# Kernel optimization log

Measured on AMD Instinct MI355X. Metric: run time of the kernel, lower is better.

Reference implementation:

```python
import jax, jax.numpy as jnp
import numpy as np

B, N, DIM, H = 8, 1024, 512, 8
D = DIM // H
SCALE = DIM ** -0.5


def setup_inputs() -> dict:
    key = jax.random.key(0)
    ks = jax.random.split(key, 8)
    s = 0.02
    return {
        "x": jax.random.normal(ks[0], (B, N, DIM), dtype=jnp.float32),
        "mask": jax.random.uniform(ks[1], (1, 1, N, N), dtype=jnp.float32),
        "Wqkv1": jax.random.normal(ks[2], (DIM, 3 * DIM), dtype=jnp.float32) * s,
        "bqkv1": jnp.zeros((3 * DIM,), dtype=jnp.float32),
        "Wqkv2": jax.random.normal(ks[3], (DIM, 3 * DIM), dtype=jnp.float32) * s,
        "bqkv2": jnp.zeros((3 * DIM,), dtype=jnp.float32),
        "Wnn1": jax.random.normal(ks[4], (DIM, DIM), dtype=jnp.float32) * s,
        "bnn1": jnp.zeros((DIM,), dtype=jnp.float32),
    }


def _split_heads(qkv, b, n):
    # qkv: [b, n, 3*dim] -> three [b, h, n, d]
    q, k, v = jnp.split(qkv, 3, axis=-1)
    r = lambda t: t.reshape(b, n, H, D).transpose(0, 2, 1, 3)
    return r(q), r(k), r(v)


def reference(x, mask, Wqkv1, bqkv1, Wqkv2, bqkv2, Wnn1, bnn1):
    b, n, dim = x.shape
    # Stage 1: mask-scaled sigmoid attention (no softmax, no scale)
    q, k, v = _split_heads(x @ Wqkv1 + bqkv1, b, n)
    dots = jax.nn.sigmoid(jnp.einsum('bhid,bhjd->bhij', q, k) * mask)
    out1 = jnp.einsum('bhij,bhjd->bhid', dots, v)
    out1 = out1.transpose(0, 2, 1, 3).reshape(b, n, dim)
    # Stage 2: standard scaled softmax attention on stage-1 output
    q, k, v = _split_heads(out1 @ Wqkv2 + bqkv2, b, n)
    attn = jax.nn.softmax(jnp.einsum('bhid,bhjd->bhij', q, k) * SCALE, axis=-1)
    out = jnp.einsum('bhij,bhjd->bhid', attn, v)
    out = out.transpose(0, 2, 1, 3).reshape(b, n, dim)
    # Output projection (dropout is identity in eval mode)
    return out @ Wnn1 + bnn1
```

## Files before the change

### kernel.cpp

```cpp
#include <hip/hip_runtime.h>
#include <hip/hip_bf16.h>
#include <stdint.h>

constexpr int B_ = 8, N_ = 1024, DIM_ = 512, H_ = 8, D_ = 64;
constexpr int BH_ = B_ * H_;
constexpr int M_  = B_ * N_;
constexpr float SCALE_ = 0.04419417382415922f;
constexpr float LOG2E_ = 1.44269504088896f;
constexpr float QSL2E_ = SCALE_ * LOG2E_;

typedef __bf16 bf16x8 __attribute__((ext_vector_type(8)));
typedef float  f32x4  __attribute__((ext_vector_type(4)));
typedef unsigned short u16;
typedef u16 u16x8 __attribute__((ext_vector_type(8)));
typedef u16 u16x4 __attribute__((ext_vector_type(4)));

static __device__ __forceinline__ u16 f2bf(float f) {
  return __builtin_bit_cast(u16, (__bf16)f);
}
static __device__ __forceinline__ bf16x8 ld8(const u16* p) {
  return __builtin_bit_cast(bf16x8, *reinterpret_cast<const u16x8*>(p));
}
static __device__ __forceinline__ f32x4 mfma16(bf16x8 a, bf16x8 b, f32x4 c) {
  return __builtin_amdgcn_mfma_f32_16x16x32_bf16(a, b, c, 0, 0, 0);
}
static __device__ __forceinline__ void gload_lds16(const u16* g, void* l) {
  __builtin_amdgcn_global_load_lds(
      (const __attribute__((address_space(1))) void*)g,
      (__attribute__((address_space(3))) void*)l, 16, 0, 0);
}

__global__ void k_cvt(const float* __restrict__ in, u16* __restrict__ out, int n4) {
  int i = blockIdx.x * blockDim.x + threadIdx.x;
  int stride = gridDim.x * blockDim.x;
  for (int idx = i; idx < n4; idx += stride) {
    float4 v = reinterpret_cast<const float4*>(in)[idx];
    u16x4 o;
    o[0] = f2bf(v.x); o[1] = f2bf(v.y); o[2] = f2bf(v.z); o[3] = f2bf(v.w);
    reinterpret_cast<u16x4*>(out)[idx] = o;
  }
}

__global__ void k_mask(const float* __restrict__ in, float* __restrict__ out, int n4) {
  int i = blockIdx.x * blockDim.x + threadIdx.x;
  int stride = gridDim.x * blockDim.x;
  for (int idx = i; idx < n4; idx += stride) {
    float4 v = reinterpret_cast<const float4*>(in)[idx];
    v.x *= -LOG2E_; v.y *= -LOG2E_; v.z *= -LOG2E_; v.w *= -LOG2E_;
    reinterpret_cast<float4*>(out)[idx] = v;
  }
}

__global__ void k_wt(const float* __restrict__ W, u16* __restrict__ Wt, int ncols, float qs) {
  int idx = blockIdx.x * 256 + threadIdx.x;
  if (idx >= ncols * 512) return;
  int c = idx >> 9, k = idx & 511;
  float v = W[k * ncols + c];
  if (c < 512) v *= qs;
  Wt[idx] = f2bf(v);
}

template<int NC, int MODE, bool SQ>
__global__ __launch_bounds__(256) void k_gemm(
    const u16* __restrict__ A, const u16* __restrict__ Wt, const float* __restrict__ bias,
    u16* __restrict__ qo, u16* __restrict__ ko, u16* __restrict__ vto, float* __restrict__ fo)
{
  __shared__ __attribute__((aligned(16))) u16 As[2][128 * 32];
  __shared__ __attribute__((aligned(16))) u16 Bs[2][128 * 32];
  const int wv = threadIdx.x >> 6, ln = threadIdx.x & 63;
  const int lr = ln & 15, lg = ln >> 4;
  const int wr = wv >> 1, wc = wv & 1;
  const int r0 = blockIdx.x * 128;
  const int c0 = blockIdx.y * 128;

  auto stage = [&](int bufi, int kk) {
#pragma unroll
    for (int q = 0; q < 2; ++q) {
      int L = (wv * 2 + q) * 1024 + ln * 16;
      int row = L >> 6;
      int col = ((L & 63) ^ (((row >> 1) & 3) << 4)) >> 1;
      gload_lds16(A  + (size_t)(r0 + row) * 512 + kk + col, (char*)As[bufi] + (wv * 2 + q) * 1024);
      gload_lds16(Wt + (size_t)(c0 + row) * 512 + kk + col, (char*)Bs[bufi] + (wv * 2 + q) * 1024);
    }
  };
  auto swzld = [&](const u16* tile, int row, int colb) -> bf16x8 {
    int byte = (row << 6) + (colb ^ (((row >> 1) & 3) << 4));
    return __builtin_bit_cast(bf16x8, *reinterpret_cast<const u16x8*>((const char*)tile + byte));
  };

  f32x4 acc[4][4] = {};
  stage(0, 0);
  int buf = 0;
  for (int kk = 0; kk < 512; kk += 32) {
    __syncthreads();
    if (kk + 32 < 512) stage(buf ^ 1, kk + 32);
    bf16x8 af[4], bfb[4];
#pragma unroll
    for (int m = 0; m < 4; ++m) af[m]  = swzld(As[buf], wr * 64 + m * 16 + lr, lg * 16);
#pragma unroll
    for (int n = 0; n < 4; ++n) bfb[n] = swzld(Bs[buf], wc * 64 + n * 16 + lr, lg * 16);
#pragma unroll
    for (int m = 0; m < 4; ++m)
#pragma unroll
      for (int n = 0; n < 4; ++n)
        acc[m][n] = mfma16(af[m], bfb[n], acc[m][n]);
    buf ^= 1;
  }

#pragma unroll
  for (int m = 0; m < 4; ++m)
#pragma unroll
    for (int n = 0; n < 4; ++n) {
      const int gc  = c0 + wc * 64 + n * 16 + lr;
      const int gr0 = r0 + wr * 64 + m * 16 + lg * 4;
      const float bsc = (SQ && gc < 512) ? QSL2E_ : 1.f;
      const float bv = bias[gc] * bsc;
      if (MODE == 0) {
        const int part = gc >> 9, cc = gc & 511;
        const int hh = cc >> 6, dd = cc & 63;
        const int bb = gr0 >> 10, nn = gr0 & 1023;
        const int bh = bb * H_ + hh;
        if (part == 2) {
          u16x4 w;
#pragma unroll
          for (int r = 0; r < 4; ++r) w[r] = f2bf(acc[m][n][r] + bv);
          *reinterpret_cast<u16x4*>(&vto[((size_t)(bh * D_ + dd)) * N_ + nn]) = w;
        } else {
          u16* dst = (part == 0 ? qo : ko) + ((size_t)(bh * N_ + nn)) * D_ + dd;
#pragma unroll
          for (int r = 0; r < 4; ++r) dst[(size_t)r * D_] = f2bf(acc[m][n][r] + bv);
        }
      } else {
#pragma unroll
        for (int r = 0; r < 4; ++r)
          fo[(size_t)(gr0 + r) * NC + gc] = acc[m][n][r] + bv;
      }
    }
}

template<int STAGE>
__global__ __launch_bounds__(512, 4) void k_attn(
    const u16* __restrict__ Q, const u16* __restrict__ K, const u16* __restrict__ Vt,
    const float* __restrict__ mask, u16* __restrict__ O)
{
  __shared__ __attribute__((aligned(16))) u16 Kb[2][64 * 64];
  __shared__ __attribute__((aligned(16))) u16 Vb[2][64 * 64];
  __shared__ __attribute__((aligned(16))) u16 pbuf[8][16][72];
  const int wv = threadIdx.x >> 6, ln = threadIdx.x & 63;
  const int lr = ln & 15, lg = ln >> 4;
  const int bh = blockIdx.y;
  const int i0 = blockIdx.x * 128 + wv * 16;
  const size_t base = (size_t)bh * N_ * D_;

  auto stageKV = [&](int bufi, int jt2) {
    int L = wv * 1024 + ln * 16;
    int row = L >> 7;
    int col = ((L & 127) ^ ((row & 7) << 4)) >> 1;
    gload_lds16(K  + base + (size_t)(jt2 + row) * 64 + col,  (char*)Kb[bufi] + wv * 1024);
    gload_lds16(Vt + base + (size_t)row * 1024 + jt2 + col,  (char*)Vb[bufi] + wv * 1024);
  };
  auto swzld = [&](const u16* tile, int row, int colb) -> bf16x8 {
    int byte = (row << 7) + (colb ^ ((row & 7) << 4));
    return __builtin_bit_cast(bf16x8, *reinterpret_cast<const u16x8*>((const char*)tile + byte));
  };

  bf16x8 aq0 = ld8(Q + base + (size_t)(i0 + lr) * D_ + lg * 8);
  bf16x8 aq1 = ld8(Q + base + (size_t)(i0 + lr) * D_ + 32 + lg * 8);

  f32x4 acco[4] = {};
  float ssum_ln = 0.f;

  float4 mk[4];
  const float* mrow = mask + (size_t)(i0 + lr) * N_;
  auto loadmask = [&](int jt2) {
#pragma unroll
    for (int js = 0; js < 4; ++js)
      mk[js] = *reinterpret_cast<const float4*>(&mrow[jt2 + js * 16 + lg * 4]);
  };
  if (STAGE == 1) loadmask(0);

  stageKV(0, 0);
  int buf = 0;
  for (int jt = 0; jt < N_; jt += 64) {
    __syncthreads();
    if (jt + 64 < N_) stageKV(buf ^ 1, jt + 64);

    f32x4 s[4];
    __builtin_amdgcn_s_setprio(1);
#pragma unroll
    for (int js = 0; js < 4; ++js) {
      int krow = js * 16 + lr;
      bf16x8 bk0 = swzld(Kb[buf], krow, lg * 16);
      bf16x8 bk1 = swzld(Kb[buf], krow, 64 + lg * 16);
      f32x4 z = {};
      z = mfma16(bk0, aq0, z);
      z = mfma16(bk1, aq1, z);
      s[js] = z;
    }
    __builtin_amdgcn_s_setprio(0);

    if (STAGE == 1) {
#pragma unroll
      for (int js = 0; js < 4; ++js) {
        u16x4 w;
#pragma unroll
        for (int r = 0; r < 4; ++r) {
          float mkr = (r == 0) ? mk[js].x : (r == 1) ? mk[js].y : (r == 2) ? mk[js].z : mk[js].w;
          float e = exp2f(s[js][r] * mkr);
          w[r] = f2bf(__builtin_amdgcn_rcpf(1.f + e));
        }
        *reinterpret_cast<u16x4*>(&pbuf[wv][lr][js * 16 + lg * 4]) = w;
      }
      if (jt + 64 < N_) loadmask(jt + 64);
    } else {
      float ps = 0.f;
#pragma unroll
      for (int js = 0; js < 4; ++js) {
        u16x4 w;
#pragma unroll
        for (int r = 0; r < 4; ++r) {
          float p = exp2f(s[js][r]);
          ps += p;
          w[r] = f2bf(p);
        }
        *reinterpret_cast<u16x4*>(&pbuf[wv][lr][js * 16 + lg * 4]) = w;
      }
      ssum_ln += ps;
    }

    bf16x8 ap0 = ld8(&pbuf[wv][lr][lg * 8]);
    bf16x8 ap1 = ld8(&pbuf[wv][lr][32 + lg * 8]);
    __builtin_amdgcn_s_setprio(1);
#pragma unroll
    for (int db = 0; db < 4; ++db) {
      bf16x8 bv0 = swzld(Vb[buf], db * 16 + lr, lg * 16);
      bf16x8 bv1 = swzld(Vb[buf], db * 16 + lr, 64 + lg * 16);
      acco[db] = mfma16(ap1, bv1, mfma16(ap0, bv0, acco[db]));
    }
    __builtin_amdgcn_s_setprio(0);
    buf ^= 1;
  }

  float inv[4];
  if (STAGE == 2) {
    float st = ssum_ln;
    st += __shfl_xor(st, 16);
    st += __shfl_xor(st, 32);
#pragma unroll
    for (int r = 0; r < 4; ++r)
      inv[r] = __builtin_amdgcn_rcpf(__shfl(st, lg * 4 + r));
  }

#pragma unroll
  for (int db = 0; db < 4; ++db)
#pragma unroll
    for (int r = 0; r < 4; ++r) {
      float v = acco[db][r];
      if (STAGE == 2) v *= inv[r];
      pbuf[wv][lg * 4 + r][db * 16 + lr] = f2bf(v);
    }
  bf16x8 o0v = ld8(&pbuf[wv][lr][lg * 8]);
  bf16x8 o1v = ld8(&pbuf[wv][lr][32 + lg * 8]);
  const int bb = bh >> 3, hh = bh & 7;
  u16* orow = O + (size_t)(bb * N_ + i0 + lr) * DIM_ + hh * D_;
  *reinterpret_cast<u16x8*>(orow + lg * 8)      = __builtin_bit_cast(u16x8, o0v);
  *reinterpret_cast<u16x8*>(orow + 32 + lg * 8) = __builtin_bit_cast(u16x8, o1v);
}

extern "C" void kernel_launch(void* const* d_in, const int* in_sizes, int n_in,
                              void* d_out, int out_size, void* d_ws, size_t ws_size,
                              hipStream_t stream)
{
  const float* x    = (const float*)d_in[0];
  const float* mask = (const float*)d_in[1];
  const float* W1   = (const float*)d_in[2];
  const float* b1   = (const float*)d_in[3];
  const float* W2   = (const float*)d_in[4];
  const float* b2   = (const float*)d_in[5];
  const float* W3   = (const float*)d_in[6];
  const float* b3   = (const float*)d_in[7];
  float* out = (float*)d_out;

  char* ws = (char*)d_ws;
  size_t off = 0;
  auto alloc = [&](size_t bytes) { char* p = ws + off; off += (bytes + 255) & ~255ULL; return p; };
  u16*   W1t = (u16*)alloc((size_t)1536 * 512 * 2);
  u16*   W2t = (u16*)alloc((size_t)1536 * 512 * 2);
  u16*   W3t = (u16*)alloc((size_t)512 * 512 * 2);
  u16*   xb  = (u16*)alloc((size_t)M_ * DIM_ * 2);
  u16*   q   = (u16*)alloc((size_t)BH_ * N_ * D_ * 2);
  u16*   k   = (u16*)alloc((size_t)BH_ * N_ * D_ * 2);
  u16*   vt  = (u16*)alloc((size_t)BH_ * N_ * D_ * 2);
  u16*   o1  = (u16*)alloc((size_t)M_ * DIM_ * 2);
  float* mk  = (float*)alloc((size_t)N_ * N_ * 4);
  u16*   o2  = xb;

  k_cvt<<<2048, 256, 0, stream>>>(x, xb, M_ * DIM_ / 4);
  k_mask<<<1024, 256, 0, stream>>>(mask, mk, N_ * N_ / 4);
  k_wt<<<(1536 * 512 + 255) / 256, 256, 0, stream>>>(W1, W1t, 1536, 1.f);
  k_wt<<<(1536 * 512 + 255) / 256, 256, 0, stream>>>(W2, W2t, 1536, QSL2E_);
  k_wt<<<(512 * 512 + 255) / 256, 256, 0, stream>>>(W3, W3t, 512, 1.f);

  dim3 g1(M_ / 128, 1536 / 128);
  k_gemm<1536, 0, false><<<g1, 256, 0, stream>>>(xb, W1t, b1, q, k, vt, nullptr);

  dim3 ga(N_ / 128, BH_);
  k_attn<1><<<ga, 512, 0, stream>>>(q, k, vt, mk, o1);

  k_gemm<1536, 0, true><<<g1, 256, 0, stream>>>(o1, W2t, b2, q, k, vt, nullptr);

  k_attn<2><<<ga, 512, 0, stream>>>(q, k, vt, mk, o2);

  dim3 g3(M_ / 128, 512 / 128);
  k_gemm<512, 1, false><<<g3, 256, 0, stream>>>(o2, W3t, b3, nullptr, nullptr, nullptr, out);
}
```

Before: 228.5 us.

## Fuse prep kernels into one launch with tiled weight transpose and GEMM block swizzle

Replaces the five preprocessing launches (x conversion, mask scaling, three weight transposes) with one kernel whose block ranges handle each job. The weight transpose now goes through a padded 64x64 shared-memory tile, so global reads and writes are coalesced instead of strided. The GEMM also remaps block indices with an XCD-style swizzle so that neighbouring blocks share A/B tiles in cache. The swizzle hardcodes 64 row tiles (M/128), which holds for every GEMM launch here.

Result: no change. 225.3 us (-1.4%).

```diff
diff --git a/kernel.cpp b/kernel.cpp
--- a/kernel.cpp
+++ b/kernel.cpp
@@ -30,34 +30,52 @@
       (__attribute__((address_space(3))) void*)l, 16, 0, 0);
 }
 
-__global__ void k_cvt(const float* __restrict__ in, u16* __restrict__ out, int n4) {
-  int i = blockIdx.x * blockDim.x + threadIdx.x;
-  int stride = gridDim.x * blockDim.x;
-  for (int idx = i; idx < n4; idx += stride) {
-    float4 v = reinterpret_cast<const float4*>(in)[idx];
-    u16x4 o;
-    o[0] = f2bf(v.x); o[1] = f2bf(v.y); o[2] = f2bf(v.z); o[3] = f2bf(v.w);
-    reinterpret_cast<u16x4*>(out)[idx] = o;
+__global__ __launch_bounds__(256) void k_prep(
+    const float* __restrict__ x, const float* __restrict__ mask,
+    const float* __restrict__ W1, const float* __restrict__ W2,
+    const float* __restrict__ W3,
+    u16* __restrict__ xb, float* __restrict__ mk,
+    u16* __restrict__ W1t, u16* __restrict__ W2t, u16* __restrict__ W3t)
+{
+  __shared__ float fl[64][65];
+  const int b = blockIdx.x, t = threadIdx.x;
+  if (b < 4096) {
+    int idx = b * 256 + t;
+    float4 v = reinterpret_cast<const float4*>(x)[idx];
+    u16x4 o; o[0] = f2bf(v.x); o[1] = f2bf(v.y); o[2] = f2bf(v.z); o[3] = f2bf(v.w);
+    reinterpret_cast<u16x4*>(xb)[idx] = o;
+  } else if (b < 5120) {
+    int idx = (b - 4096) * 256 + t;
+    float4 v = reinterpret_cast<const float4*>(mask)[idx];
+    v.x *= -LOG2E_; v.y *= -LOG2E_; v.z *= -LOG2E_; v.w *= -LOG2E_;
+    reinterpret_cast<float4*>(mk)[idx] = v;
+  } else {
+    int tb = b - 5120;
+    const float* Ws; u16* Wd; int NC, kt, ct; bool isW2 = false;
+    if (tb < 192)      { Ws = W1; Wd = W1t; NC = 1536; kt = tb / 24; ct = tb % 24; }
+    else if (tb < 384) { tb -= 192; Ws = W2; Wd = W2t; NC = 1536; kt = tb / 24; ct = tb % 24; isW2 = true; }
+    else               { tb -= 384; Ws = W3; Wd = W3t; NC = 512;  kt = tb >> 3; ct = tb & 7; }
+    const int tr = t >> 4, tc = t & 15;
+#pragma unroll
+    for (int i = 0; i < 4; ++i) {
+      int row = i * 16 + tr;
+      float4 v = *reinterpret_cast<const float4*>(
+          &Ws[(size_t)(kt * 64 + row) * NC + ct * 64 + tc * 4]);
+      fl[row][tc * 4 + 0] = v.x; fl[row][tc * 4 + 1] = v.y;
+      fl[row][tc * 4 + 2] = v.z; fl[row][tc * 4 + 3] = v.w;
+    }
+    __syncthreads();
+#pragma unroll
+    for (int i = 0; i < 4; ++i) {
+      int wr = i * 16 + tr;
+      int c = ct * 64 + wr;
+      float sc = (isW2 && c < 512) ? QSL2E_ : 1.f;
+      u16x4 w;
+#pragma unroll
+      for (int e = 0; e < 4; ++e) w[e] = f2bf(fl[tc * 4 + e][wr] * sc);
+      *reinterpret_cast<u16x4*>(&Wd[(size_t)c * 512 + kt * 64 + tc * 4]) = w;
+    }
   }
-}
-
-__global__ void k_mask(const float* __restrict__ in, float* __restrict__ out, int n4) {
-  int i = blockIdx.x * blockDim.x + threadIdx.x;
-  int stride = gridDim.x * blockDim.x;
-  for (int idx = i; idx < n4; idx += stride) {
-    float4 v = reinterpret_cast<const float4*>(in)[idx];
-    v.x *= -LOG2E_; v.y *= -LOG2E_; v.z *= -LOG2E_; v.w *= -LOG2E_;
-    reinterpret_cast<float4*>(out)[idx] = v;
-  }
-}
-
-__global__ void k_wt(const float* __restrict__ W, u16* __restrict__ Wt, int ncols, float qs) {
-  int idx = blockIdx.x * 256 + threadIdx.x;
-  if (idx >= ncols * 512) return;
-  int c = idx >> 9, k = idx & 511;
-  float v = W[k * ncols + c];
-  if (c < 512) v *= qs;
-  Wt[idx] = f2bf(v);
 }
 
 template<int NC, int MODE, bool SQ>
@@ -70,8 +88,11 @@
   const int wv = threadIdx.x >> 6, ln = threadIdx.x & 63;
   const int lr = ln & 15, lg = ln >> 4;
   const int wr = wv >> 1, wc = wv & 1;
-  const int r0 = blockIdx.x * 128;
-  const int c0 = blockIdx.y * 128;
+  const int nwg = gridDim.x * gridDim.y;
+  const int lin = blockIdx.y * gridDim.x + blockIdx.x;
+  const int swz = (lin & 7) * (nwg >> 3) + (lin >> 3);
+  const int r0 = (swz & 63) * 128;
+  const int c0 = (swz >> 6) * 128;
 
   auto stage = [&](int bufi, int kk) {
 #pragma unroll
@@ -295,11 +316,7 @@
   float* mk  = (float*)alloc((size_t)N_ * N_ * 4);
   u16*   o2  = xb;
 
-  k_cvt<<<2048, 256, 0, stream>>>(x, xb, M_ * DIM_ / 4);
-  k_mask<<<1024, 256, 0, stream>>>(mask, mk, N_ * N_ / 4);
-  k_wt<<<(1536 * 512 + 255) / 256, 256, 0, stream>>>(W1, W1t, 1536, 1.f);
-  k_wt<<<(1536 * 512 + 255) / 256, 256, 0, stream>>>(W2, W2t, 1536, QSL2E_);
-  k_wt<<<(512 * 512 + 255) / 256, 256, 0, stream>>>(W3, W3t, 512, 1.f);
+  k_prep<<<5568, 256, 0, stream>>>(x, mask, W1, W2, W3, xb, mk, W1t, W2t, W3t);
 
   dim3 g1(M_ / 128, 1536 / 128);
   k_gemm<1536, 0, false><<<g1, 256, 0, stream>>>(xb, W1t, b1, q, k, vt, nullptr);
```
